# Kernel tuning notes

Measured on AMD Instinct MI355X. Metric: run time of the kernel, lower is better.

The kernel has to match this reference:

```python
import jax, jax.numpy as jnp
import numpy as np

N_HEADS = 8
D_MODEL = 256
HEAD_DEPTH = D_MODEL // N_HEADS
B, S = 2, 4096


def setup_inputs() -> dict:
    key = jax.random.key(0)
    ks = jax.random.split(key, 8)
    scale = 1.0 / np.sqrt(D_MODEL)
    return {
        "q": jax.random.normal(ks[0], (B, S, D_MODEL), dtype=jnp.float32),
        "k": jax.random.normal(ks[1], (B, S, D_MODEL), dtype=jnp.float32),
        "v": jax.random.normal(ks[2], (B, S, D_MODEL), dtype=jnp.float32),
        "mask": jax.random.randint(ks[3], (B, S, S), 0, 2).astype(jnp.bool_),
        "wq": jax.random.normal(ks[4], (D_MODEL, D_MODEL), dtype=jnp.float32) * scale,
        "wk": jax.random.normal(ks[5], (D_MODEL, D_MODEL), dtype=jnp.float32) * scale,
        "wv": jax.random.normal(ks[6], (D_MODEL, D_MODEL), dtype=jnp.float32) * scale,
        "w_out": jax.random.normal(ks[7], (D_MODEL, D_MODEL), dtype=jnp.float32) * scale,
    }


def _split_heads(x):
    # [B, S, D] -> [B, H, S, Dh]
    b, s, _ = x.shape
    return x.reshape(b, s, N_HEADS, HEAD_DEPTH).transpose(0, 2, 1, 3)


def reference(q, k, v, mask, wq, wk, wv, w_out):
    Q = _split_heads(q @ wq)
    K = _split_heads(k @ wk)
    V = _split_heads(v @ wv)
    # [B, H, Sq, Sk]
    scores = jnp.einsum('bhqd,bhkd->bhqk', Q, K) / jnp.sqrt(
        jnp.asarray(HEAD_DEPTH, dtype=Q.dtype))
    # mask True -> -inf, broadcast over heads
    scores = jnp.where(mask[:, None, :, :], -jnp.inf, scores)
    probs = jax.nn.softmax(scores, axis=-1)
    attn = jnp.einsum('bhqk,bhkd->bhqd', probs, V)
    attn = attn.transpose(0, 2, 1, 3).reshape(q.shape[0], -1, D_MODEL)
    return attn @ w_out
```

## Files before the change

kernel.cpp:

```cpp
#include <hip/hip_runtime.h>
#include <stdint.h>

typedef __bf16 bf16;
typedef __bf16 bf16x8 __attribute__((ext_vector_type(8)));
typedef __bf16 bf16x4 __attribute__((ext_vector_type(4)));
typedef float  f32x2  __attribute__((ext_vector_type(2)));
typedef float  f32x4  __attribute__((ext_vector_type(4)));
typedef float  f32x16 __attribute__((ext_vector_type(16)));
typedef float  float4v __attribute__((ext_vector_type(4)));
typedef int    int4v   __attribute__((ext_vector_type(4)));
typedef unsigned int uint;
typedef unsigned long long ull;

#define QSCALE 0.25505003984214403f


__global__ __launch_bounds__(256) void transpose_w(
    const float* __restrict__ w0, const float* __restrict__ w1,
    const float* __restrict__ w2, const float* __restrict__ w3,
    bf16* __restrict__ WT) {
  const int wsel = blockIdx.z;
  const float* W = wsel == 0 ? w0 : wsel == 1 ? w1 : wsel == 2 ? w2 : w3;
  const int k0 = blockIdx.x * 64, n0 = blockIdx.y * 64;
  __shared__ __align__(16) bf16 t[64][72];
  const int tid = threadIdx.x;
  {
    const int kk = (tid >> 4) << 2;
    const int nn = (tid & 15) << 2;
#pragma unroll
    for (int r = 0; r < 4; ++r) {
      float4v a = *(const float4v*)(W + (size_t)(k0 + kk + r) * 256 + n0 + nn);
#pragma unroll
      for (int j = 0; j < 4; ++j) t[nn + j][kk + r] = (bf16)a[j];
    }
  }
  __syncthreads();
  {
    const int ni = tid >> 2;
    const int c  = (tid & 3) * 16;
    bf16x8 o0 = *(const bf16x8*)(&t[ni][c]);
    bf16x8 o1 = *(const bf16x8*)(&t[ni][c + 8]);
    bf16* dst = WT + (size_t)wsel * 65536 + (size_t)(n0 + ni) * 256 + k0 + c;
    *(bf16x8*)dst = o0;
    *(bf16x8*)(dst + 8) = o1;
  }
}

__global__ __launch_bounds__(256) void proj_pack(
    const float* __restrict__ xq, const float* __restrict__ xk, const float* __restrict__ xv,
    const bf16* __restrict__ WT,
    bf16* __restrict__ Qp, bf16* __restrict__ Kp, bf16* __restrict__ Vp,
    const int* __restrict__ mask, uint* __restrict__ M2) {
  __shared__ __align__(16) unsigned char smem[18432];
  const int tid = threadIdx.x;

  if (blockIdx.x < 1024) {
    uint* trans = (uint*)smem;
    const int pid = blockIdx.x;
    const int bb = pid >> 9;
    const int qt = (pid >> 2) & 127;
    const int kc = pid & 3;
    const int q0 = qt * 32;
    const int w = tid >> 6, l = tid & 63;
    const int d2 = l & 7;
    const int sh = 8 * d2;
#pragma unroll 4
    for (int t = 0; t < 32; ++t) {
      const int q_l = w * 8 + (t >> 2), c = t & 3;
      const int4v m = *(const int4v*)(mask + ((size_t)(bb * 4096 + q0 + q_l)) * 4096 +
                                      kc * 1024 + c * 256 + 4 * l);
      uint out = 0;
#pragma unroll
      for (int i = 0; i < 4; ++i) {
        ull b = __ballot(m[i] != 0);
        out |= ((uint)(b >> sh) & 0xFFu) << (8 * i);
      }
      if (l < 8) trans[(c * 8 + d2) * 36 + q_l] = out;
    }
    __syncthreads();
    {
      const int r = tid >> 3, c4 = (tid & 7) * 4;
      int4v a = *(const int4v*)(trans + r * 36 + c4);
      *(int4v*)(M2 + ((size_t)(bb * 128 + kc * 32 + r)) * 4096 + q0 + c4) = a;
    }
    return;
  }

  const int pb = blockIdx.x - 1024;
  const int z = pb >> 8;
  const int r8 = pb & 255;
  const int m0 = (r8 >> 1) * 64, n0 = (r8 & 1) * 128;
  const float* X = z == 0 ? xq : (z == 1 ? xk : xv);
  const bf16* wt = WT + (size_t)z * 65536;
  const int wave = tid >> 6, lane = tid & 63;
  const int nl = lane & 15, quad = lane >> 4;
  const int arow = m0 + wave * 16 + nl;
  const float* xrow = X + (size_t)arow * 256;

  f32x4 zero4 = {0.f, 0.f, 0.f, 0.f};
  f32x4 acc[8];
#pragma unroll
  for (int i = 0; i < 8; ++i) acc[i] = zero4;

  for (int ks = 0; ks < 8; ++ks) {
    float4v a0 = *(const float4v*)(xrow + ks * 32 + quad * 8);
    float4v a1 = *(const float4v*)(xrow + ks * 32 + quad * 8 + 4);
    bf16x8 af;
#pragma unroll
    for (int i = 0; i < 4; ++i) { af[i] = (bf16)a0[i]; af[4 + i] = (bf16)a1[i]; }
#pragma unroll
    for (int nf = 0; nf < 8; ++nf) {
      bf16x8 bfr = *(const bf16x8*)(wt + (size_t)(n0 + nf * 16 + nl) * 256 + ks * 32 + quad * 8);
      acc[nf] = __builtin_amdgcn_mfma_f32_16x16x32_bf16(af, bfr, acc[nf], 0, 0, 0);
    }
  }

  const int bq = m0 >> 12;
  const int s0 = m0 & 4095;
  const int posl = wave * 16 + quad * 4;

  if (z == 2) {
    bf16* tv = (bf16*)smem;
#pragma unroll
    for (int nf = 0; nf < 8; ++nf) {
      const int col = nf * 16 + nl;
      bf16x4 o;
#pragma unroll
      for (int rr = 0; rr < 4; ++rr) o[rr] = (bf16)acc[nf][rr];
      *(bf16x4*)(tv + (size_t)col * 72 + posl) = o;
    }
    __syncthreads();
    const int h2 = tid >> 6, ln = tid & 63;
    const int d = ln & 31, shalf = ln >> 5;
    const int h = (n0 >> 5) + h2;
    bf16* vb = Vp + (size_t)(bq * 8 + h) * 131072 + (size_t)(s0 >> 5) * 1024 + d * 8;
#pragma unroll
    for (int it = 0; it < 4; ++it) {
      const int blk = it >> 1, sub = (it & 1) * 2 + shalf;
      const int K0 = (sub >> 1) * 16 + (sub & 1) * 4;
      const bf16* src = tv + (size_t)(h2 * 32 + d) * 72 + blk * 32 + K0;
      bf16x4 g0 = *(const bf16x4*)(src);
      bf16x4 g1 = *(const bf16x4*)(src + 8);
      bf16x8 o;
#pragma unroll
      for (int j = 0; j < 4; ++j) { o[j] = g0[j]; o[4 + j] = g1[j]; }
      *(bf16x8*)(vb + (size_t)blk * 1024 + sub * 256) = o;
    }
  } else {
    bf16* tq = (bf16*)smem;
    const float scale = (z == 0) ? QSCALE : 1.0f;
#pragma unroll
    for (int nf = 0; nf < 8; ++nf) {
      const int col = nf * 16 + nl;
#pragma unroll
      for (int rr = 0; rr < 4; ++rr)
        tq[(size_t)(posl + rr) * 136 + col] = (bf16)(acc[nf][rr] * scale);
    }
    __syncthreads();
    bf16* Out = z == 0 ? Qp : Kp;
    const int h2 = tid >> 6, ln = tid & 63;
    const int h = (n0 >> 5) + h2;
    const int s = s0 + ln;
    bf16* ob = Out + (size_t)(bq * 8 + h) * 131072 + (size_t)(s >> 5) * 1024 + (s & 31) * 8;
#pragma unroll
    for (int sub = 0; sub < 4; ++sub) {
      bf16x8 o = *(const bf16x8*)(tq + (size_t)ln * 136 + h2 * 32 + sub * 8);
      *(bf16x8*)(ob + sub * 256) = o;
    }
  }
}

__global__ __launch_bounds__(256) void attn_kernel(
    const bf16* __restrict__ Qp, const bf16* __restrict__ Kp,
    const bf16* __restrict__ Vp, const uint* __restrict__ M2,
    bf16* __restrict__ Og) {
  const int id = blockIdx.x;
  const int xcd = id & 7, slot = id >> 3;
  const int bh = xcd * 2 + (slot >> 6);
  const int q0 = (slot & 63) * 64;
  const int b = bh >> 3, h = bh & 7;
  const int tid = threadIdx.x, w = tid >> 6, lane = tid & 63;
  const int nl = lane & 31, half = lane >> 5;

  __shared__ float Ored[4][32][66];
  __shared__ float Lsum[64][8];

  const size_t bhbase = (size_t)bh * 131072;
  const int so0 = half * 256 + nl * 8;
  const int so1 = 512 + half * 256 + nl * 8;

  bf16x8 qf[2][2];
#pragma unroll
  for (int qt = 0; qt < 2; ++qt) {
    const bf16* qb = Qp + bhbase + (size_t)((q0 >> 5) + qt) * 1024;
    qf[qt][0] = *(const bf16x8*)(qb + so0);
    qf[qt][1] = *(const bf16x8*)(qb + so1);
  }

  const bf16* Kw = Kp + bhbase + (size_t)w * 1024;
  const bf16* Vw = Vp + bhbase + (size_t)w * 1024;
  const uint* Mw = M2 + (size_t)b * 524288 + (size_t)w * 4096 + q0 + nl;

  f32x16 z16;
#pragma unroll
  for (int i = 0; i < 16; ++i) z16[i] = 0.f;
  f32x16 acc0 = z16, acc1 = z16;
  f32x2 ls0 = {0.f, 0.f}, ls1 = {0.f, 0.f};

  struct Frag { bf16x8 ka0, ka1, va0, va1; uint m0, m1; };
  auto LOADF = [&](int kt) -> Frag {
    Frag f;
    const bf16* kc = Kw + (size_t)kt * 4096;
    const bf16* vc = Vw + (size_t)kt * 4096;
    f.ka0 = *(const bf16x8*)(kc + so0);
    f.ka1 = *(const bf16x8*)(kc + so1);
    f.va0 = *(const bf16x8*)(vc + so0);
    f.va1 = *(const bf16x8*)(vc + so1);
    const uint* mp = Mw + (size_t)kt * 16384;
    f.m0 = mp[0];
    f.m1 = mp[32];
    return f;
  };

  auto STEP = [&](const Frag& f) {
    const int minv0 = (int)((~f.m0) >> half);
    const int minv1 = (int)((~f.m1) >> half);
    f32x16 st0 = __builtin_amdgcn_mfma_f32_32x32x16_bf16(f.ka0, qf[0][0], z16, 0, 0, 0);
    st0 = __builtin_amdgcn_mfma_f32_32x32x16_bf16(f.ka1, qf[0][1], st0, 0, 0, 0);
    f32x16 st1 = __builtin_amdgcn_mfma_f32_32x32x16_bf16(f.ka0, qf[1][0], z16, 0, 0, 0);
    st1 = __builtin_amdgcn_mfma_f32_32x32x16_bf16(f.ka1, qf[1][1], st1, 0, 0, 0);

    f32x16 pf0, pf1;
#pragma unroll
    for (int g = 0; g < 4; ++g)
#pragma unroll
      for (int r = 0; r < 4; ++r) {
        const int i = g * 4 + r, off = 8 * r + 2 * g;
        float e0 = __builtin_amdgcn_exp2f(st0[i]);
        float e1 = __builtin_amdgcn_exp2f(st1[i]);
        const uint k0m = (uint)__builtin_amdgcn_sbfe(minv0, off, 1);
        const uint k1m = (uint)__builtin_amdgcn_sbfe(minv1, off, 1);
        e0 = __uint_as_float(__float_as_uint(e0) & k0m);
        e1 = __uint_as_float(__float_as_uint(e1) & k1m);
        pf0[i] = e0; pf1[i] = e1;
      }
#pragma unroll
    for (int i = 0; i < 16; i += 2) {
      f32x2 a0 = {pf0[i], pf0[i + 1]};
      f32x2 a1 = {pf1[i], pf1[i + 1]};
      ls0 += a0; ls1 += a1;
    }
    const bf16x8 pb00 = __builtin_convertvector(
        __builtin_shufflevector(pf0, pf0, 0, 1, 2, 3, 4, 5, 6, 7), bf16x8);
    const bf16x8 pb01 = __builtin_convertvector(
        __builtin_shufflevector(pf0, pf0, 8, 9, 10, 11, 12, 13, 14, 15), bf16x8);
    const bf16x8 pb10 = __builtin_convertvector(
        __builtin_shufflevector(pf1, pf1, 0, 1, 2, 3, 4, 5, 6, 7), bf16x8);
    const bf16x8 pb11 = __builtin_convertvector(
        __builtin_shufflevector(pf1, pf1, 8, 9, 10, 11, 12, 13, 14, 15), bf16x8);

    acc0 = __builtin_amdgcn_mfma_f32_32x32x16_bf16(f.va0, pb00, acc0, 0, 0, 0);
    acc0 = __builtin_amdgcn_mfma_f32_32x32x16_bf16(f.va1, pb01, acc0, 0, 0, 0);
    acc1 = __builtin_amdgcn_mfma_f32_32x32x16_bf16(f.va0, pb10, acc1, 0, 0, 0);
    acc1 = __builtin_amdgcn_mfma_f32_32x32x16_bf16(f.va1, pb11, acc1, 0, 0, 0);
  };

  Frag fa = LOADF(0), fb;
  for (int kt = 0; kt < 32; kt += 2) {
    fb = LOADF(kt + 1);
    STEP(fa);
    if (kt + 2 < 32) fa = LOADF(kt + 2);
    STEP(fb);
  }

#pragma unroll
  for (int g = 0; g < 4; ++g)
#pragma unroll
    for (int r = 0; r < 4; ++r) {
      const int d = r + 8 * g + 4 * half, i = g * 4 + r;
      Ored[w][d][nl] = acc0[i];
      Ored[w][d][32 + nl] = acc1[i];
    }
  Lsum[nl][w * 2 + half] = ls0.x + ls0.y;
  Lsum[32 + nl][w * 2 + half] = ls1.x + ls1.y;
  __syncthreads();
  if (tid < 64) {
    float s = 0.f;
#pragma unroll
    for (int j = 0; j < 8; ++j) s += Lsum[tid][j];
    Lsum[tid][0] = 1.0f / s;
  }
  __syncthreads();
  {
    const int q = tid >> 2, db = (tid & 3) * 8;
    const float rl = Lsum[q][0];
    bf16x8 o;
#pragma unroll
    for (int dj = 0; dj < 8; ++dj) {
      const float s = Ored[0][db + dj][q] + Ored[1][db + dj][q] +
                      Ored[2][db + dj][q] + Ored[3][db + dj][q];
      o[dj] = (bf16)(s * rl);
    }
    *(bf16x8*)(Og + ((size_t)(b * 4096 + q0 + q)) * 256 + h * 32 + db) = o;
  }
}

__global__ __launch_bounds__(256) void gemm_out(
    const bf16* __restrict__ A, const bf16* __restrict__ WTo, float* __restrict__ C) {
  const int m0 = blockIdx.x * 64, n0 = blockIdx.y * 64;
  const int tid = threadIdx.x, wave = tid >> 6, lane = tid & 63;
  const int nl = lane & 15, quad = lane >> 4;
  const int arow = m0 + wave * 16 + nl;

  f32x4 zero4 = {0.f, 0.f, 0.f, 0.f};
  f32x4 acc[4];
#pragma unroll
  for (int i = 0; i < 4; ++i) acc[i] = zero4;

  for (int ks = 0; ks < 8; ++ks) {
    bf16x8 af = *(const bf16x8*)(A + (size_t)arow * 256 + ks * 32 + quad * 8);
#pragma unroll
    for (int nf = 0; nf < 4; ++nf) {
      bf16x8 bfr = *(const bf16x8*)(WTo + (size_t)(n0 + nf * 16 + nl) * 256 + ks * 32 + quad * 8);
      acc[nf] = __builtin_amdgcn_mfma_f32_16x16x32_bf16(af, bfr, acc[nf], 0, 0, 0);
    }
  }
  const int Rbase = m0 + wave * 16 + quad * 4;
#pragma unroll
  for (int nf = 0; nf < 4; ++nf)
#pragma unroll
    for (int r = 0; r < 4; ++r)
      C[(size_t)(Rbase + r) * 256 + n0 + nf * 16 + nl] = acc[nf][r];
}

extern "C" void kernel_launch(void* const* d_in, const int* in_sizes, int n_in,
                              void* d_out, int out_size, void* d_ws, size_t ws_size,
                              hipStream_t stream) {
  const float* q  = (const float*)d_in[0];
  const float* k  = (const float*)d_in[1];
  const float* v  = (const float*)d_in[2];
  const int*  mask = (const int*)d_in[3];
  const float* wq = (const float*)d_in[4];
  const float* wk = (const float*)d_in[5];
  const float* wv = (const float*)d_in[6];
  const float* wo = (const float*)d_in[7];
  float* out = (float*)d_out;

  uint8_t* ws = (uint8_t*)d_ws;
  bf16* WT = (bf16*)ws;
  bf16* Qp = (bf16*)(ws + (512u << 10));
  bf16* Kp = Qp + 2097152;
  bf16* Vp = Kp + 2097152;
  uint* Mb = (uint*)((uint8_t*)(Vp + 2097152));
  bf16* Ao = (bf16*)((uint8_t*)Mb + (4u << 20));

  transpose_w<<<dim3(4, 4, 4), 256, 0, stream>>>(wq, wk, wv, wo, WT);
  proj_pack<<<dim3(1024 + 768), 256, 0, stream>>>(q, k, v, WT, Qp, Kp, Vp, mask, Mb);
  attn_kernel<<<dim3(1024), 256, 0, stream>>>(Qp, Kp, Vp, Mb, Ao);
  gemm_out<<<dim3(128, 4), 256, 0, stream>>>(Ao, WT + 3 * 65536, out);
}
```

Before: 336.8 us.

## Split attention by query rows per wave, compute row sums via MFMA

The attention kernel now gives each of two waves its own 32 query rows and loops over all 128 key tiles, where before four waves split the keys and their partial outputs were reduced in shared memory. This drops the large cross-wave reduction buffer and one barrier. The softmax denominator now comes from an extra MFMA against a ones vector, and probabilities are packed to bf16 with a byte permute instead of a vector convert. The mask-packing loop is also batched so eight loads are issued before the ballots. In exchange, each wave runs a longer serial loop, the block is smaller and carries an occupancy hint, and the MFMA count per step rises.

Result: no change. 333.9 us (-0.9%).

```diff
diff --git a/kernel.cpp b/kernel.cpp
--- a/kernel.cpp
+++ b/kernel.cpp
@@ -2,14 +2,15 @@
 #include <stdint.h>
 
 typedef __bf16 bf16;
+typedef __bf16 bf16x2 __attribute__((ext_vector_type(2)));
+typedef __bf16 bf16x4 __attribute__((ext_vector_type(4)));
 typedef __bf16 bf16x8 __attribute__((ext_vector_type(8)));
-typedef __bf16 bf16x4 __attribute__((ext_vector_type(4)));
-typedef float  f32x2  __attribute__((ext_vector_type(2)));
 typedef float  f32x4  __attribute__((ext_vector_type(4)));
 typedef float  f32x16 __attribute__((ext_vector_type(16)));
 typedef float  float4v __attribute__((ext_vector_type(4)));
 typedef int    int4v   __attribute__((ext_vector_type(4)));
 typedef unsigned int uint;
+typedef uint   uint4v  __attribute__((ext_vector_type(4)));
 typedef unsigned long long ull;
 
 #define QSCALE 0.25505003984214403f
@@ -64,18 +65,27 @@
     const int w = tid >> 6, l = tid & 63;
     const int d2 = l & 7;
     const int sh = 8 * d2;
-#pragma unroll 4
-    for (int t = 0; t < 32; ++t) {
-      const int q_l = w * 8 + (t >> 2), c = t & 3;
-      const int4v m = *(const int4v*)(mask + ((size_t)(bb * 4096 + q0 + q_l)) * 4096 +
-                                      kc * 1024 + c * 256 + 4 * l);
-      uint out = 0;
-#pragma unroll
-      for (int i = 0; i < 4; ++i) {
-        ull b = __ballot(m[i] != 0);
-        out |= ((uint)(b >> sh) & 0xFFu) << (8 * i);
+    for (int batch = 0; batch < 4; ++batch) {
+      int4v m[8];
+#pragma unroll
+      for (int u = 0; u < 8; ++u) {
+        const int q_l = w * 8 + batch * 2 + (u >> 2);
+        const int c = u & 3;
+        m[u] = *(const int4v*)(mask + ((size_t)(bb * 4096 + q0 + q_l)) * 4096 +
+                               kc * 1024 + c * 256 + 4 * l);
       }
-      if (l < 8) trans[(c * 8 + d2) * 36 + q_l] = out;
+#pragma unroll
+      for (int u = 0; u < 8; ++u) {
+        const int q_l = w * 8 + batch * 2 + (u >> 2);
+        const int c = u & 3;
+        uint out = 0;
+#pragma unroll
+        for (int i = 0; i < 4; ++i) {
+          ull b = __ballot(m[u][i] != 0);
+          out |= ((uint)(b >> sh) & 0xFFu) << (8 * i);
+        }
+        if (l < 8) trans[(c * 8 + d2) * 36 + q_l] = out;
+      }
     }
     __syncthreads();
     {
@@ -170,138 +180,114 @@
   }
 }
 
-__global__ __launch_bounds__(256) void attn_kernel(
+__global__ __launch_bounds__(128, 3) void attn_kernel(
     const bf16* __restrict__ Qp, const bf16* __restrict__ Kp,
     const bf16* __restrict__ Vp, const uint* __restrict__ M2,
     bf16* __restrict__ Og) {
   const int id = blockIdx.x;
   const int xcd = id & 7, slot = id >> 3;
   const int bh = xcd * 2 + (slot >> 6);
-  const int q0 = (slot & 63) * 64;
+  const int qt = slot & 63;
   const int b = bh >> 3, h = bh & 7;
   const int tid = threadIdx.x, w = tid >> 6, lane = tid & 63;
   const int nl = lane & 31, half = lane >> 5;
 
-  __shared__ float Ored[4][32][66];
-  __shared__ float Lsum[64][8];
+  __shared__ __align__(16) bf16 T[64][40];
 
   const size_t bhbase = (size_t)bh * 131072;
   const int so0 = half * 256 + nl * 8;
   const int so1 = 512 + half * 256 + nl * 8;
-
-  bf16x8 qf[2][2];
-#pragma unroll
-  for (int qt = 0; qt < 2; ++qt) {
-    const bf16* qb = Qp + bhbase + (size_t)((q0 >> 5) + qt) * 1024;
-    qf[qt][0] = *(const bf16x8*)(qb + so0);
-    qf[qt][1] = *(const bf16x8*)(qb + so1);
-  }
-
-  const bf16* Kw = Kp + bhbase + (size_t)w * 1024;
-  const bf16* Vw = Vp + bhbase + (size_t)w * 1024;
-  const uint* Mw = M2 + (size_t)b * 524288 + (size_t)w * 4096 + q0 + nl;
+  const int qg = qt * 64 + w * 32;
+
+  const bf16* qb = Qp + bhbase + (size_t)(qg >> 5) * 1024;
+  const bf16x8 qf0 = *(const bf16x8*)(qb + so0);
+  const bf16x8 qf1 = *(const bf16x8*)(qb + so1);
+
+  const bf16* Kb = Kp + bhbase;
+  const bf16* Vb = Vp + bhbase;
+  const uint* Mb = M2 + (size_t)b * 524288 + qg + nl;
 
   f32x16 z16;
 #pragma unroll
   for (int i = 0; i < 16; ++i) z16[i] = 0.f;
-  f32x16 acc0 = z16, acc1 = z16;
-  f32x2 ls0 = {0.f, 0.f}, ls1 = {0.f, 0.f};
-
-  struct Frag { bf16x8 ka0, ka1, va0, va1; uint m0, m1; };
-  auto LOADF = [&](int kt) -> Frag {
+  f32x16 acc = z16, lacc = z16;
+  bf16x8 ones;
+#pragma unroll
+  for (int i = 0; i < 8; ++i) ones[i] = (bf16)1.0f;
+
+  struct Frag { bf16x8 ka0, ka1, va0, va1; uint m; };
+  auto LOADF = [&](int kdw) -> Frag {
     Frag f;
-    const bf16* kc = Kw + (size_t)kt * 4096;
-    const bf16* vc = Vw + (size_t)kt * 4096;
+    const bf16* kc = Kb + (size_t)kdw * 1024;
+    const bf16* vc = Vb + (size_t)kdw * 1024;
     f.ka0 = *(const bf16x8*)(kc + so0);
     f.ka1 = *(const bf16x8*)(kc + so1);
     f.va0 = *(const bf16x8*)(vc + so0);
     f.va1 = *(const bf16x8*)(vc + so1);
-    const uint* mp = Mw + (size_t)kt * 16384;
-    f.m0 = mp[0];
-    f.m1 = mp[32];
+    f.m = Mb[(size_t)kdw * 4096];
     return f;
   };
 
   auto STEP = [&](const Frag& f) {
-    const int minv0 = (int)((~f.m0) >> half);
-    const int minv1 = (int)((~f.m1) >> half);
-    f32x16 st0 = __builtin_amdgcn_mfma_f32_32x32x16_bf16(f.ka0, qf[0][0], z16, 0, 0, 0);
-    st0 = __builtin_amdgcn_mfma_f32_32x32x16_bf16(f.ka1, qf[0][1], st0, 0, 0, 0);
-    f32x16 st1 = __builtin_amdgcn_mfma_f32_32x32x16_bf16(f.ka0, qf[1][0], z16, 0, 0, 0);
-    st1 = __builtin_amdgcn_mfma_f32_32x32x16_bf16(f.ka1, qf[1][1], st1, 0, 0, 0);
-
-    f32x16 pf0, pf1;
+    const int minv = (int)((~f.m) >> half);
+    f32x16 st = __builtin_amdgcn_mfma_f32_32x32x16_bf16(f.ka0, qf0, z16, 0, 0, 0);
+    st = __builtin_amdgcn_mfma_f32_32x32x16_bf16(f.ka1, qf1, st, 0, 0, 0);
+
+    uint pk[8];
 #pragma unroll
     for (int g = 0; g < 4; ++g)
 #pragma unroll
-      for (int r = 0; r < 4; ++r) {
-        const int i = g * 4 + r, off = 8 * r + 2 * g;
-        float e0 = __builtin_amdgcn_exp2f(st0[i]);
-        float e1 = __builtin_amdgcn_exp2f(st1[i]);
-        const uint k0m = (uint)__builtin_amdgcn_sbfe(minv0, off, 1);
-        const uint k1m = (uint)__builtin_amdgcn_sbfe(minv1, off, 1);
-        e0 = __uint_as_float(__float_as_uint(e0) & k0m);
-        e1 = __uint_as_float(__float_as_uint(e1) & k1m);
-        pf0[i] = e0; pf1[i] = e1;
+      for (int rp = 0; rp < 2; ++rp) {
+        const int i = g * 4 + rp * 2;
+        float e0 = __builtin_amdgcn_exp2f(st[i]);
+        float e1 = __builtin_amdgcn_exp2f(st[i + 1]);
+        const uint k0m = (uint)__builtin_amdgcn_sbfe(minv, 8 * (2 * rp) + 2 * g, 1);
+        const uint k1m = (uint)__builtin_amdgcn_sbfe(minv, 8 * (2 * rp + 1) + 2 * g, 1);
+        const uint u0 = __float_as_uint(e0) & k0m;
+        const uint u1 = __float_as_uint(e1) & k1m;
+        pk[g * 2 + rp] = __builtin_amdgcn_perm(u1, u0, 0x07060302u);
       }
-#pragma unroll
-    for (int i = 0; i < 16; i += 2) {
-      f32x2 a0 = {pf0[i], pf0[i + 1]};
-      f32x2 a1 = {pf1[i], pf1[i + 1]};
-      ls0 += a0; ls1 += a1;
-    }
-    const bf16x8 pb00 = __builtin_convertvector(
-        __builtin_shufflevector(pf0, pf0, 0, 1, 2, 3, 4, 5, 6, 7), bf16x8);
-    const bf16x8 pb01 = __builtin_convertvector(
-        __builtin_shufflevector(pf0, pf0, 8, 9, 10, 11, 12, 13, 14, 15), bf16x8);
-    const bf16x8 pb10 = __builtin_convertvector(
-        __builtin_shufflevector(pf1, pf1, 0, 1, 2, 3, 4, 5, 6, 7), bf16x8);
-    const bf16x8 pb11 = __builtin_convertvector(
-        __builtin_shufflevector(pf1, pf1, 8, 9, 10, 11, 12, 13, 14, 15), bf16x8);
-
-    acc0 = __builtin_amdgcn_mfma_f32_32x32x16_bf16(f.va0, pb00, acc0, 0, 0, 0);
-    acc0 = __builtin_amdgcn_mfma_f32_32x32x16_bf16(f.va1, pb01, acc0, 0, 0, 0);
-    acc1 = __builtin_amdgcn_mfma_f32_32x32x16_bf16(f.va0, pb10, acc1, 0, 0, 0);
-    acc1 = __builtin_amdgcn_mfma_f32_32x32x16_bf16(f.va1, pb11, acc1, 0, 0, 0);
+    uint4v a0 = {pk[0], pk[1], pk[2], pk[3]};
+    uint4v a1 = {pk[4], pk[5], pk[6], pk[7]};
+    const bf16x8 pb0 = __builtin_bit_cast(bf16x8, a0);
+    const bf16x8 pb1 = __builtin_bit_cast(bf16x8, a1);
+
+    acc  = __builtin_amdgcn_mfma_f32_32x32x16_bf16(f.va0, pb0, acc, 0, 0, 0);
+    lacc = __builtin_amdgcn_mfma_f32_32x32x16_bf16(ones,  pb0, lacc, 0, 0, 0);
+    acc  = __builtin_amdgcn_mfma_f32_32x32x16_bf16(f.va1, pb1, acc, 0, 0, 0);
+    lacc = __builtin_amdgcn_mfma_f32_32x32x16_bf16(ones,  pb1, lacc, 0, 0, 0);
   };
 
   Frag fa = LOADF(0), fb;
-  for (int kt = 0; kt < 32; kt += 2) {
-    fb = LOADF(kt + 1);
+  for (int kdw = 0; kdw < 128; kdw += 2) {
+    fb = LOADF(kdw + 1);
     STEP(fa);
-    if (kt + 2 < 32) fa = LOADF(kt + 2);
+    if (kdw + 2 < 128) fa = LOADF(kdw + 2);
     STEP(fb);
   }
 
+  const float rl = 1.0f / lacc[0];
 #pragma unroll
   for (int g = 0; g < 4; ++g)
 #pragma unroll
-    for (int r = 0; r < 4; ++r) {
-      const int d = r + 8 * g + 4 * half, i = g * 4 + r;
-      Ored[w][d][nl] = acc0[i];
-      Ored[w][d][32 + nl] = acc1[i];
-    }
-  Lsum[nl][w * 2 + half] = ls0.x + ls0.y;
-  Lsum[32 + nl][w * 2 + half] = ls1.x + ls1.y;
-  __syncthreads();
-  if (tid < 64) {
-    float s = 0.f;
-#pragma unroll
-    for (int j = 0; j < 8; ++j) s += Lsum[tid][j];
-    Lsum[tid][0] = 1.0f / s;
-  }
+    for (int rp = 0; rp < 2; ++rp) {
+      const int i = g * 4 + rp * 2;
+      const int d = rp * 2 + 8 * g + 4 * half;
+      bf16x2 o;
+      o[0] = (bf16)(acc[i] * rl);
+      o[1] = (bf16)(acc[i + 1] * rl);
+      *(bf16x2*)(&T[w * 32 + nl][d]) = o;
+    }
   __syncthreads();
   {
-    const int q = tid >> 2, db = (tid & 3) * 8;
-    const float rl = Lsum[q][0];
-    bf16x8 o;
-#pragma unroll
-    for (int dj = 0; dj < 8; ++dj) {
-      const float s = Ored[0][db + dj][q] + Ored[1][db + dj][q] +
-                      Ored[2][db + dj][q] + Ored[3][db + dj][q];
-      o[dj] = (bf16)(s * rl);
-    }
-    *(bf16x8*)(Og + ((size_t)(b * 4096 + q0 + q)) * 256 + h * 32 + db) = o;
+    const int ql = tid & 63, rep = tid >> 6;
+    bf16* obase = Og + ((size_t)(b * 4096 + qt * 64 + ql)) * 256 + h * 32;
+#pragma unroll
+    for (int c = 0; c < 2; ++c) {
+      const int chunk = rep * 2 + c;
+      bf16x8 o = *(const bf16x8*)(&T[ql][chunk * 8]);
+      *(bf16x8*)(obase + chunk * 8) = o;
+    }
   }
 }
 
@@ -356,6 +342,6 @@
 
   transpose_w<<<dim3(4, 4, 4), 256, 0, stream>>>(wq, wk, wv, wo, WT);
   proj_pack<<<dim3(1024 + 768), 256, 0, stream>>>(q, k, v, WT, Qp, Kp, Vp, mask, Mb);
-  attn_kernel<<<dim3(1024), 256, 0, stream>>>(Qp, Kp, Vp, Mb, Ao);
+  attn_kernel<<<dim3(1024), 128, 0, stream>>>(Qp, Kp, Vp, Mb, Ao);
   gemm_out<<<dim3(128, 4), 256, 0, stream>>>(Ao, WT + 3 * 65536, out);
 }
```
